# Kernel optimization log

Measured on AMD Instinct MI355X. Metric: run time of the kernel, lower is better.

The kernel has to match this reference:

```python
import jax, jax.numpy as jnp
import numpy as np

# --- static config (mirrors init_kwargs) ---
B, N, CBEV = 4, 4, 64
D, FH, FW = 41, 16, 44          # depth bins, feature H/W after downsample
OGH, OGW, DS = 256, 704, 16     # original image dims, downsample
NX, NY, NZ = 240, 240, 1        # BEV grid (x, y, z)
DX = np.array([0.4, 0.4, 20.0], np.float32)            # voxel size
BX = np.array([-47.8, -47.8, 0.0], np.float32)          # voxel grid origin (bound+dx/2)


def _frustum():
    # [D, FH, FW, 3] with (u_pixel, v_pixel, depth); UD discretization 4..44 step 1
    ds = (4.0 + np.arange(D, dtype=np.float32)).reshape(D, 1, 1) * np.ones((1, FH, FW), np.float32)
    xs = np.linspace(0.0, OGW - 1, FW, dtype=np.float32).reshape(1, 1, FW) * np.ones((D, FH, 1), np.float32)
    ys = np.linspace(0.0, OGH - 1, FH, dtype=np.float32).reshape(1, FH, 1) * np.ones((D, 1, FW), np.float32)
    return jnp.asarray(np.stack([xs, ys, ds], axis=-1))


def setup_inputs() -> dict:
    key = jax.random.key(0)
    x = jax.random.normal(key, (B, N, D, FH, FW, CBEV), dtype=jnp.float32)
    # realistic camera rig: 4 cameras at yaw 0/90/180/270 deg, pinhole intrinsics
    intr = np.zeros((N, 3, 3), np.float32)
    rot = np.zeros((N, 3, 3), np.float32)
    tr = np.zeros((N, 3), np.float32)
    cam2ego = np.array([[0, 0, 1], [-1, 0, 0], [0, -1, 0]], np.float32)  # cam z-fwd -> ego x-fwd
    for n in range(N):
        intr[n] = np.array([[500.0, 0.0, OGW / 2.0], [0.0, 500.0, OGH / 2.0], [0.0, 0.0, 1.0]], np.float32)
        yaw = 2.0 * np.pi * n / N
        c, s = np.cos(yaw), np.sin(yaw)
        Rz = np.array([[c, -s, 0], [s, c, 0], [0, 0, 1]], np.float32)
        rot[n] = Rz @ cam2ego
        tr[n] = np.array([1.5 * c, 1.5 * s, 1.6], np.float32)
    rots = jnp.asarray(np.broadcast_to(rot, (B, N, 3, 3)).copy())
    trans = jnp.asarray(np.broadcast_to(tr, (B, N, 3)).copy())
    intrins = jnp.asarray(np.broadcast_to(intr, (B, N, 3, 3)).copy())
    post_rots = jnp.asarray(np.broadcast_to(np.eye(3, dtype=np.float32), (B, N, 3, 3)).copy())
    post_trans = jnp.zeros((B, N, 3), jnp.float32)
    return {"x": x, "rots": rots, "trans": trans, "intrins": intrins,
            "post_rots": post_rots, "post_trans": post_trans}


def reference(x, rots, trans, intrins, post_rots, post_trans):
    # --- get_geometry: frustum pixel/depth points -> ego-frame xyz ---
    frustum = _frustum()                                            # [D,FH,FW,3]
    pts = frustum[None, None] - post_trans[:, :, None, None, None, :]
    pts = jnp.einsum('bnij,bndhwj->bndhwi', jnp.linalg.inv(post_rots), pts)
    pts = jnp.concatenate([pts[..., :2] * pts[..., 2:3], pts[..., 2:3]], axis=-1)
    combine = rots @ jnp.linalg.inv(intrins)
    pts = jnp.einsum('bnij,bndhwj->bndhwi', combine, pts) + trans[:, :, None, None, None, :]
    # --- voxel_pooling: quantize, mask OOB, segment-sum into dense BEV grid ---
    dx = jnp.asarray(DX)
    bx = jnp.asarray(BX)
    vox = ((pts - (bx - dx / 2.0)) / dx).astype(jnp.int32)          # trunc, same as torch .long()
    vx, vy, vz = vox[..., 0], vox[..., 1], vox[..., 2]              # [B,N,D,FH,FW]
    kept = (vx >= 0) & (vx < NX) & (vy >= 0) & (vy < NY) & (vz >= 0) & (vz < NZ)
    bidx = jnp.arange(B, dtype=jnp.int32)[:, None, None, None, None]
    nvox = B * NZ * NY * NX
    lin = bidx * (NZ * NY * NX) + vz * (NY * NX) + vy * NX + vx
    lin = jnp.where(kept, lin, nvox).reshape(-1)                    # invalid -> dummy bin
    feats = x.reshape(-1, CBEV)                                     # [Nprime, C]
    sums = jax.ops.segment_sum(feats, lin, num_segments=nvox + 1)[:nvox]
    final = sums.reshape(B, NZ, NY, NX, CBEV).transpose(0, 1, 4, 2, 3)  # [B,Z,C,Y,X]
    # torch: cat(final.unbind(dim=2), 1) on [B,C,Z,Y,X] -> [B, Z*C, Y, X] z-major
    return final.reshape(B, NZ * CBEV, NY, NX)
```

## Files before the change

kernel.cpp:

```cpp
#include <hip/hip_runtime.h>

#define BB   4
#define NNC  4
#define DDEP 41
#define FHH  16
#define FWW  44
#define CC   64
#define NXX  240
#define NYY  240
#define NVOX (BB*NYY*NXX)
#define NTRI (BB*NNC*DDEP*FWW)
#define SLOTS 8

#define W_CNT  0
#define W_TAB  (NVOX)

__device__ __forceinline__ void inv3x3_upper_f32(const float K[9], float o[9]) {
    float a00 = __fdiv_rn(1.0f, K[0]);
    float a11 = __fdiv_rn(1.0f, K[4]);
    float a22 = __fdiv_rn(1.0f, K[8]);
    float b01 = __fmul_rn(-a11, __fmul_rn(a00, K[1]));
    float x0 = __fadd_rn(__fmul_rn(a00, K[2]), __fmul_rn(b01, K[5]));
    float x1 = __fmul_rn(a11, K[5]);
    float b02 = __fmul_rn(-a22, x0);
    float b12 = __fmul_rn(-a22, x1);
    o[0]=a00; o[1]=b01; o[2]=b02;
    o[3]=0.0f; o[4]=a11; o[5]=b12;
    o[6]=0.0f; o[7]=0.0f; o[8]=a22;
}

__global__ void __launch_bounds__(256) geom(
        const float* __restrict__ rots,
        const float* __restrict__ trans,
        const float* __restrict__ intrins,
        const float* __restrict__ post_rots,
        const float* __restrict__ post_trans,
        unsigned int* __restrict__ cntp,
        unsigned int* __restrict__ table) {
    int wid  = threadIdx.x >> 6;
    int lane = threadIdx.x & 63;
    int sub  = lane >> 4;
    int h    = lane & 15;
    int tri  = (blockIdx.x*4 + wid)*4 + sub;

    int w    = tri % FWW;
    int rest = tri / FWW;
    int d    = rest % DDEP;
    int bn   = rest / DDEP;

    float K[9], PR[9], R[9];
    #pragma unroll
    for (int i = 0; i < 9; ++i) {
        K[i]  = intrins[bn*9 + i];
        PR[i] = post_rots[bn*9 + i];
        R[i]  = rots[bn*9 + i];
    }
    float Ki[9], PRi[9];
    inv3x3_upper_f32(K, Ki);
    inv3x3_upper_f32(PR, PRi);
    float C[9];
    #pragma unroll
    for (int i = 0; i < 3; ++i)
        #pragma unroll
        for (int j = 0; j < 3; ++j) {
            float s = __fmul_rn(R[i*3+0], Ki[0*3+j]);
            s = __fadd_rn(s, __fmul_rn(R[i*3+1], Ki[1*3+j]));
            s = __fadd_rn(s, __fmul_rn(R[i*3+2], Ki[2*3+j]));
            C[i*3+j] = s;
        }
    float ptx = post_trans[bn*3+0], pty = post_trans[bn*3+1], ptz = post_trans[bn*3+2];
    float trx = trans[bn*3+0], try_ = trans[bn*3+1], trz = trans[bn*3+2];

    float u  = (float)((double)w * (703.0/43.0));
    float v  = (float)((double)h * 17.0);
    float dd = (float)(4 + d);

    float p0x = __fsub_rn(u,  ptx);
    float p0y = __fsub_rn(v,  pty);
    float p0z = __fsub_rn(dd, ptz);
    float p1x = __fadd_rn(__fadd_rn(__fmul_rn(PRi[0],p0x), __fmul_rn(PRi[1],p0y)), __fmul_rn(PRi[2],p0z));
    float p1y = __fadd_rn(__fadd_rn(__fmul_rn(PRi[3],p0x), __fmul_rn(PRi[4],p0y)), __fmul_rn(PRi[5],p0z));
    float p1z = __fadd_rn(__fadd_rn(__fmul_rn(PRi[6],p0x), __fmul_rn(PRi[7],p0y)), __fmul_rn(PRi[8],p0z));
    float p2x = __fmul_rn(p1x, p1z);
    float p2y = __fmul_rn(p1y, p1z);
    float p2z = p1z;
    float ex = __fadd_rn(__fadd_rn(__fmul_rn(C[0],p2x), __fmul_rn(C[1],p2y)), __fmul_rn(C[2],p2z));
    float ey = __fadd_rn(__fadd_rn(__fmul_rn(C[3],p2x), __fmul_rn(C[4],p2y)), __fmul_rn(C[5],p2z));
    float ez = __fadd_rn(__fadd_rn(__fmul_rn(C[6],p2x), __fmul_rn(C[7],p2y)), __fmul_rn(C[8],p2z));
    float gx = __fadd_rn(ex, trx);
    float gy = __fadd_rn(ey, try_);
    float gz = __fadd_rn(ez, trz);

    float qx = __fdiv_rn(__fsub_rn(gx, -48.0f), 0.4f);
    float qy = __fdiv_rn(__fsub_rn(gy, -48.0f), 0.4f);
    float qz = __fdiv_rn(__fsub_rn(gz, -10.0f), 20.0f);
    int vx = (int)qx;
    int vy = (int)qy;
    int vz = (int)qz;

    bool kept = (vx >= 0) & (vx < NXX) & (vy >= 0) & (vy < NYY) & (vz == 0);
    unsigned long long bal = __ballot(kept);
    unsigned int mask = (unsigned int)((bal >> (sub*16)) & 0xFFFFull);

    if (h == 0 && mask != 0) {
        int b  = bn / NNC;
        int vb = b*(NYY*NXX) + vy*NXX + vx;
        unsigned int sh  = 8u*(vb & 3);
        unsigned int old = atomicAdd(&cntp[vb >> 2], 1u << sh);
        unsigned int sl  = (old >> sh) & 0xFFu;
        if (sl < SLOTS) table[vb*SLOTS + sl] = ((unsigned int)tri << 16) | mask;
    }
}

__global__ void __launch_bounds__(256) assemble(
        const float* __restrict__ x,
        const unsigned int* __restrict__ cntp,
        const unsigned int* __restrict__ table,
        float* __restrict__ out) {
    __shared__ float lds[16*65];
    int tid  = threadIdx.x;
    int wid  = tid >> 6;
    int lane = tid & 63;
    int v0   = blockIdx.x*16;

    unsigned int cw = cntp[(v0 >> 2) + wid];

    #pragma unroll
    for (int k = 0; k < 4; ++k) {
        int cell = v0 + wid*4 + k;
        int n = (int)((cw >> (8*k)) & 0xFFu); if (n > SLOTS) n = SLOTS;
        unsigned int ent = (lane < n) ? table[cell*SLOTS + lane] : 0u;
        float a[8];
        #pragma unroll
        for (int q = 0; q < 8; ++q) a[q] = 0.0f;
        int j = 0;
        for (int i = 0; i < n; ++i) {
            unsigned int e = __shfl((int)ent, i);
            int tri  = (int)(e >> 16);
            unsigned int m = e & 0xFFFFu;
            int w    = tri % FWW;
            int rest = tri / FWW;
            int d    = rest % DDEP;
            int bn   = rest / DDEP;
            const float* xb = x + (size_t)((bn*DDEP + d)*FHH*FWW + w)*CC + lane;
            if (m == 0xFFFFu) {
                #pragma unroll
                for (int hh = 0; hh < 16; ++hh)
                    a[hh & 7] += xb[(size_t)hh*(FWW*CC)];
            } else {
                while (m) {
                    int hh = __ffs(m) - 1;
                    m &= m - 1;
                    a[(j++) & 7] += xb[(size_t)hh*(FWW*CC)];
                }
            }
        }
        #pragma unroll
        for (int q = 0; q < 4; ++q) a[q] += a[q + 4];
        lds[(wid*4 + k)*65 + lane] = (a[0] + a[1]) + (a[2] + a[3]);
    }
    __syncthreads();

    int c = tid >> 2, q = tid & 3;
    float4 f;
    f.x = lds[(q*4 + 0)*65 + c];
    f.y = lds[(q*4 + 1)*65 + c];
    f.z = lds[(q*4 + 2)*65 + c];
    f.w = lds[(q*4 + 3)*65 + c];
    int b  = v0 / (NYY*NXX);
    int yx = v0 % (NYY*NXX);
    *(float4*)&out[(size_t)b*(CC*NYY*NXX) + (size_t)c*(NYY*NXX) + yx + q*4] = f;
}

extern "C" void kernel_launch(void* const* d_in, const int* in_sizes, int n_in,
                              void* d_out, int out_size, void* d_ws, size_t ws_size,
                              hipStream_t stream) {
    const float* x          = (const float*)d_in[0];
    const float* rots       = (const float*)d_in[1];
    const float* trans      = (const float*)d_in[2];
    const float* intrins    = (const float*)d_in[3];
    const float* post_rots  = (const float*)d_in[4];
    const float* post_trans = (const float*)d_in[5];
    float* out = (float*)d_out;

    char* ws = (char*)d_ws;
    unsigned int* cntp  = (unsigned int*)(ws + W_CNT);
    unsigned int* table = (unsigned int*)(ws + W_TAB);

    hipMemsetAsync(cntp, 0, NVOX, stream);
    geom<<<NTRI/16, 256, 0, stream>>>(rots, trans, intrins, post_rots, post_trans,
                                      cntp, table);
    assemble<<<NVOX/16, 256, 0, stream>>>(x, cntp, table, out);
}
```

Baseline: 235.4 us.

## Precompute per-ray height partial sums in geometry kernel, gather them in assemble

The geometry kernel now also reads the feature map for each kept (camera, depth, width) ray and writes a 64-channel partial sum over the kept height rows into a workspace buffer. The assemble kernel then sums these precomputed partials per voxel instead of gathering all 16 height rows from x. This moves the heavy feature reads into a kernel with a coalesced, ray-ordered access pattern and replaces scattered per-voxel gathers. The cost is an extra workspace write and read of one partial per kept ray.

```diff
diff --git a/kernel.cpp b/kernel.cpp
--- a/kernel.cpp
+++ b/kernel.cpp
@@ -14,6 +14,7 @@
 
 #define W_CNT  0
 #define W_TAB  (NVOX)
+#define W_PSUM (W_TAB + NVOX*SLOTS*4)
 
 __device__ __forceinline__ void inv3x3_upper_f32(const float K[9], float o[9]) {
     float a00 = __fdiv_rn(1.0f, K[0]);
@@ -29,19 +30,22 @@
     o[6]=0.0f; o[7]=0.0f; o[8]=a22;
 }
 
-__global__ void __launch_bounds__(256) geom(
+__global__ void __launch_bounds__(256) megageom(
+        const float* __restrict__ x,
         const float* __restrict__ rots,
         const float* __restrict__ trans,
         const float* __restrict__ intrins,
         const float* __restrict__ post_rots,
         const float* __restrict__ post_trans,
         unsigned int* __restrict__ cntp,
-        unsigned int* __restrict__ table) {
+        unsigned int* __restrict__ table,
+        float* __restrict__ psum) {
     int wid  = threadIdx.x >> 6;
     int lane = threadIdx.x & 63;
     int sub  = lane >> 4;
     int h    = lane & 15;
-    int tri  = (blockIdx.x*4 + wid)*4 + sub;
+    int triBase = (blockIdx.x*4 + wid)*4;
+    int tri  = triBase + sub;
 
     int w    = tri % FWW;
     int rest = tri / FWW;
@@ -100,22 +104,52 @@
 
     bool kept = (vx >= 0) & (vx < NXX) & (vy >= 0) & (vy < NYY) & (vz == 0);
     unsigned long long bal = __ballot(kept);
-    unsigned int mask = (unsigned int)((bal >> (sub*16)) & 0xFFFFull);
-
-    if (h == 0 && mask != 0) {
+
+    unsigned int mymask = (unsigned int)((bal >> (sub*16)) & 0xFFFFull);
+    if (h == 0 && mymask != 0) {
         int b  = bn / NNC;
         int vb = b*(NYY*NXX) + vy*NXX + vx;
         unsigned int sh  = 8u*(vb & 3);
         unsigned int old = atomicAdd(&cntp[vb >> 2], 1u << sh);
         unsigned int sl  = (old >> sh) & 0xFFu;
-        if (sl < SLOTS) table[vb*SLOTS + sl] = ((unsigned int)tri << 16) | mask;
+        if (sl < SLOTS) table[vb*SLOTS + sl] = ((unsigned int)tri << 16) | mymask;
+    }
+
+    #pragma unroll
+    for (int j = 0; j < 4; ++j) {
+        unsigned int m = (unsigned int)((bal >> (16*j)) & 0xFFFFull);
+        if (m == 0) continue;
+        int trij  = triBase + j;
+        int wj    = trij % FWW;
+        int restj = trij / FWW;
+        int dj    = restj % DDEP;
+        int bnj   = restj / DDEP;
+        const float* xb = x + (size_t)((bnj*DDEP + dj)*FHH*FWW + wj)*CC + lane;
+        float a[8];
+        #pragma unroll
+        for (int q = 0; q < 8; ++q) a[q] = 0.0f;
+        if (m == 0xFFFFu) {
+            #pragma unroll
+            for (int hh = 0; hh < 16; ++hh)
+                a[hh & 7] += xb[(size_t)hh*(FWW*CC)];
+        } else {
+            int jj = 0;
+            while (m) {
+                int hh = __ffs(m) - 1;
+                m &= m - 1;
+                a[(jj++) & 7] += xb[(size_t)hh*(FWW*CC)];
+            }
+        }
+        #pragma unroll
+        for (int q = 0; q < 4; ++q) a[q] += a[q + 4];
+        psum[(size_t)trij*CC + lane] = (a[0] + a[1]) + (a[2] + a[3]);
     }
 }
 
 __global__ void __launch_bounds__(256) assemble(
-        const float* __restrict__ x,
         const unsigned int* __restrict__ cntp,
         const unsigned int* __restrict__ table,
+        const float* __restrict__ psum,
         float* __restrict__ out) {
     __shared__ float lds[16*65];
     int tid  = threadIdx.x;
@@ -129,35 +163,24 @@
     for (int k = 0; k < 4; ++k) {
         int cell = v0 + wid*4 + k;
         int n = (int)((cw >> (8*k)) & 0xFFu); if (n > SLOTS) n = SLOTS;
-        unsigned int ent = (lane < n) ? table[cell*SLOTS + lane] : 0u;
-        float a[8];
-        #pragma unroll
-        for (int q = 0; q < 8; ++q) a[q] = 0.0f;
-        int j = 0;
-        for (int i = 0; i < n; ++i) {
-            unsigned int e = __shfl((int)ent, i);
-            int tri  = (int)(e >> 16);
-            unsigned int m = e & 0xFFFFu;
-            int w    = tri % FWW;
-            int rest = tri / FWW;
-            int d    = rest % DDEP;
-            int bn   = rest / DDEP;
-            const float* xb = x + (size_t)((bn*DDEP + d)*FHH*FWW + w)*CC + lane;
-            if (m == 0xFFFFu) {
-                #pragma unroll
-                for (int hh = 0; hh < 16; ++hh)
-                    a[hh & 7] += xb[(size_t)hh*(FWW*CC)];
-            } else {
-                while (m) {
-                    int hh = __ffs(m) - 1;
-                    m &= m - 1;
-                    a[(j++) & 7] += xb[(size_t)hh*(FWW*CC)];
-                }
+        float s0 = 0.0f, s1 = 0.0f, s2 = 0.0f, s3 = 0.0f;
+        if (n > 0) {
+            unsigned int ent = (lane < n) ? table[cell*SLOTS + lane] : 0u;
+            int i = 0;
+            for (; i + 4 <= n; i += 4) {
+                int t0 = __shfl((int)ent, i+0) >> 16;
+                int t1 = __shfl((int)ent, i+1) >> 16;
+                int t2 = __shfl((int)ent, i+2) >> 16;
+                int t3 = __shfl((int)ent, i+3) >> 16;
+                s0 += psum[(size_t)t0*CC + lane];
+                s1 += psum[(size_t)t1*CC + lane];
+                s2 += psum[(size_t)t2*CC + lane];
+                s3 += psum[(size_t)t3*CC + lane];
             }
+            for (; i < n; ++i)
+                s0 += psum[(size_t)(__shfl((int)ent, i) >> 16)*CC + lane];
         }
-        #pragma unroll
-        for (int q = 0; q < 4; ++q) a[q] += a[q + 4];
-        lds[(wid*4 + k)*65 + lane] = (a[0] + a[1]) + (a[2] + a[3]);
+        lds[(wid*4 + k)*65 + lane] = (s0 + s1) + (s2 + s3);
     }
     __syncthreads();
 
@@ -186,9 +209,11 @@
     char* ws = (char*)d_ws;
     unsigned int* cntp  = (unsigned int*)(ws + W_CNT);
     unsigned int* table = (unsigned int*)(ws + W_TAB);
+    float*        psum  = (float*)(ws + W_PSUM);
 
     hipMemsetAsync(cntp, 0, NVOX, stream);
-    geom<<<NTRI/16, 256, 0, stream>>>(rots, trans, intrins, post_rots, post_trans,
-                                      cntp, table);
-    assemble<<<NVOX/16, 256, 0, stream>>>(x, cntp, table, out);
-}
+    megageom<<<NTRI/16, 256, 0, stream>>>(x, rots, trans, intrins,
+                                          post_rots, post_trans,
+                                          cntp, table, psum);
+    assemble<<<NVOX/16, 256, 0, stream>>>(cntp, table, psum, out);
+}
```

New measurement: 241.4 us. +2.6%, slower.
